# Kernel optimization log

Measured on AMD Instinct MI355X. Metric: run time of the kernel, lower is better.

The kernel has to match this reference:

```python
import jax, jax.numpy as jnp
import numpy as np

N = 6144
D = 128
TAU = 0.1
ADJ_P = 0.005  # edge density


def _l2_normalize(x, eps=1e-12):
    # matches torch F.normalize: x / max(||x||, eps)
    n = jnp.sqrt(jnp.sum(x * x, axis=-1, keepdims=True))
    return x / jnp.maximum(n, eps)


def setup_inputs() -> dict:
    key = jax.random.key(0)
    ks = jax.random.split(key, 8)
    embF = jax.random.normal(ks[0], (N, D), jnp.float32)
    embM = jax.random.normal(ks[1], (N, D), jnp.float32)
    embP = jax.random.normal(ks[2], (N, D), jnp.float32)
    FM_adj = (jax.random.uniform(ks[3], (N, N)) < ADJ_P).astype(jnp.float32)
    FP_adj = (jax.random.uniform(ks[4], (N, N)) < ADJ_P).astype(jnp.float32)
    W1 = jax.random.normal(ks[5], (2 * D, D), jnp.float32) * (1.0 / np.sqrt(2 * D))
    b1 = jnp.zeros((D,), jnp.float32)
    W2 = jax.random.normal(ks[6], (D, 2), jnp.float32) * (1.0 / np.sqrt(D))
    b2 = jnp.zeros((2,), jnp.float32)
    return {"embF": embF, "embM": embM, "embP": embP,
            "FM_adj": FM_adj, "FP_adj": FP_adj,
            "W1": W1, "b1": b1, "W2": W2, "b2": b2}


def reference(embF, embM, embP, FM_adj, FP_adj, W1, b1, W2, b2):
    # attention-weighted neighbor aggregation
    FM_repr = (FM_adj @ embM) / jnp.maximum(FM_adj.sum(1, keepdims=True), 1.0)
    FP_repr = (FP_adj @ embP) / jnp.maximum(FP_adj.sum(1, keepdims=True), 1.0)
    # stack(dim=1).view(N,-1) == concat along feature dim
    feat = jnp.concatenate([FM_repr, FP_repr], axis=1)            # [N, 2D]
    h = jnp.maximum(feat @ W1 + b1, 0.0)                           # ReLU (dropout inactive in eval)
    weights = jax.nn.softmax(h @ W2 + b2, axis=-1)                 # [N, 2]

    Fn = _l2_normalize(embF)
    Mn = _l2_normalize(embM)
    Pn = _l2_normalize(embP)

    FM_sim = jnp.exp((Fn @ Mn.T) / TAU)                            # [N, Nm]
    FP_sim = jnp.exp((Fn @ Pn.T) / TAU)                            # [N, Np]

    FM_pos = jnp.sum(FM_sim * FM_adj, axis=1)
    FP_pos = jnp.sum(FP_sim * FP_adj, axis=1)
    FM_neg = jnp.sum(FM_sim, axis=1) - FM_pos
    FP_neg = jnp.sum(FP_sim, axis=1) - FP_pos

    w0, w1w = weights[:, 0], weights[:, 1]
    wp = w0 * FM_pos + w1w * FP_pos
    wn = w0 * FM_neg + w1w * FP_neg

    nei_count = jnp.maximum(FM_adj.sum(1) + FP_adj.sum(1), 1.0)
    ratio = wp / (wp + wn) / nei_count
    ratio = jnp.maximum(ratio, 1e-10)
    loss = jnp.mean(-jnp.log(ratio))
    return loss, weights
```

## Files before the change

kernel.cpp:

```cpp
#include <hip/hip_runtime.h>
#include <hip/hip_bf16.h>

#define NN 6144
#define DD 128
#define PBL 136
#define INV_TAU 10.0f

typedef __attribute__((ext_vector_type(4))) float f32x4;
typedef __attribute__((ext_vector_type(8))) short s16x8;

__device__ __forceinline__ void ld4_async(const float4* p, float4& d) {
    asm volatile("global_load_dwordx4 %0, %1, off" : "=v"(d) : "v"(p));
}
__device__ __forceinline__ void vm_wait0() {
    asm volatile("s_waitcnt vmcnt(0)" ::: "memory");
}

__global__ void k_normalize(const float* __restrict__ embF,
                            const float* __restrict__ embM,
                            const float* __restrict__ embP,
                            float* __restrict__ Fn,
                            float* __restrict__ rnM, float* __restrict__ rnP,
                            __hip_bfloat16* __restrict__ Fnb,
                            __hip_bfloat16* __restrict__ Mnb,
                            __hip_bfloat16* __restrict__ Pnb) {
    int which = blockIdx.y;
    const float* src = which == 0 ? embF : (which == 1 ? embM : embP);
    __hip_bfloat16* dstb = which == 0 ? Fnb : (which == 1 ? Mnb : Pnb);
    int wave = threadIdx.x >> 6, lane = threadIdx.x & 63;
    int row = blockIdx.x * 4 + wave;
    float2 v = reinterpret_cast<const float2*>(src + (size_t)row * DD)[lane];
    float s = v.x * v.x + v.y * v.y;
#pragma unroll
    for (int m = 1; m <= 32; m <<= 1) s += __shfl_xor(s, m);
    float inv = 1.0f / fmaxf(sqrtf(s), 1e-12f);
    float2 o; o.x = v.x * inv; o.y = v.y * inv;
    if (which == 0)
        reinterpret_cast<float2*>(Fn + (size_t)row * DD)[lane] = o;
    if (lane == 0) {
        if (which == 1) rnM[row] = inv;
        if (which == 2) rnP[row] = inv;
    }
    __hip_bfloat162 ob;
    ob.x = __float2bfloat16(o.x);
    ob.y = __float2bfloat16(o.y);
    reinterpret_cast<__hip_bfloat162*>(dstb + (size_t)row * DD)[lane] = ob;
}

__device__ __forceinline__ void sparse_body(
        int unit, char* smem,
        const float* __restrict__ FM_adj, const float* __restrict__ FP_adj,
        const float* __restrict__ embM, const float* __restrict__ embP,
        const float* __restrict__ Fn,
        const float* __restrict__ rnM, const float* __restrict__ rnP,
        float* __restrict__ feat,
        float* __restrict__ FMpos, float* __restrict__ FPpos,
        float* __restrict__ cntF, float* __restrict__ cntP) {
    float* FnS = (float*)smem;
    int (*lbufT)[4] = (int(*)[4])(smem + 512);
    int* listS = (int*)(smem + 512 + 4096);
    float (*reprS)[DD] = (float(*)[DD])(smem + 512 + 4096 + 512);
    float* posS = (float*)(smem + 512 + 4096 + 512 + 4096);
    int* wvS = (int*)(smem + 512 + 4096 + 512 + 4096 + 32);
    int* Ktot = (int*)(smem + 512 + 4096 + 512 + 4096 + 32 + 16);

    const int row = unit >> 1, h = unit & 1;
    const float* adj  = h ? FP_adj : FM_adj;
    const float* embX = h ? embP : embM;
    const float* RN   = h ? rnP : rnM;
    const int tid = threadIdx.x, wv = tid >> 6, lane = tid & 63;

    if (tid < 32)
        reinterpret_cast<float4*>(FnS)[tid] =
            reinterpret_cast<const float4*>(Fn + (size_t)row * DD)[tid];

    const float4* rp = reinterpret_cast<const float4*>(adj + (size_t)row * NN);
    float4 v0, v1, v2, v3, v4, v5;
    ld4_async(rp + tid,        v0);
    ld4_async(rp + 256 + tid,  v1);
    ld4_async(rp + 512 + tid,  v2);
    ld4_async(rp + 768 + tid,  v3);
    ld4_async(rp + 1024 + tid, v4);
    ld4_async(rp + 1280 + tid, v5);
    vm_wait0();
    float4 vv[6] = {v0, v1, v2, v3, v4, v5};
    int mycnt = 0;
#pragma unroll
    for (int u = 0; u < 6; ++u) {
        int cb = (u * 256 + tid) * 4;
        if (vv[u].x != 0.f) { if (mycnt < 4) lbufT[tid][mycnt] = cb;     mycnt++; }
        if (vv[u].y != 0.f) { if (mycnt < 4) lbufT[tid][mycnt] = cb + 1; mycnt++; }
        if (vv[u].z != 0.f) { if (mycnt < 4) lbufT[tid][mycnt] = cb + 2; mycnt++; }
        if (vv[u].w != 0.f) { if (mycnt < 4) lbufT[tid][mycnt] = cb + 3; mycnt++; }
    }
    int cnt = mycnt < 4 ? mycnt : 4;
    int x = cnt;
#pragma unroll
    for (int d = 1; d < 64; d <<= 1) {
        int y = __shfl_up(x, d);
        if (lane >= d) x += y;
    }
    int t = mycnt;
#pragma unroll
    for (int msk = 1; msk <= 32; msk <<= 1) t += __shfl_xor(t, msk);
    if (tid == 0) Ktot[1] = 0;
    if (lane == 63) wvS[wv] = x;
    __syncthreads();
    if (lane == 0) atomicAdd(&Ktot[1], t);
    if (tid == 0) {
        int s = 0;
#pragma unroll
        for (int i = 0; i < 4; ++i) { int v = wvS[i]; wvS[i] = s; s += v; }
        Ktot[0] = s < 128 ? s : 128;
    }
    __syncthreads();
    int off = wvS[wv] + (x - cnt);
    for (int i = 0; i < cnt; ++i) {
        int s = off + i;
        if (s < 128) listS[s] = lbufT[tid][i];
    }
    __syncthreads();
    const int K = Ktot[0];
    const float trueK = (float)Ktot[1];

    const int hw = tid >> 5, sl = tid & 31;
    float4 f4 = reinterpret_cast<const float4*>(FnS)[sl];
    float4 racc = {0.f, 0.f, 0.f, 0.f};
    float wsum = 0.f;
    for (int k = hw; k < K; k += 8) {
        int j = listS[k];
        float rn = RN[j];
        float4 e = reinterpret_cast<const float4*>(embX + (size_t)j * DD)[sl];
        racc.x += e.x; racc.y += e.y; racc.z += e.z; racc.w += e.w;
        float d = f4.x * e.x + f4.y * e.y + f4.z * e.z + f4.w * e.w;
#pragma unroll
        for (int msk = 1; msk <= 16; msk <<= 1) d += __shfl_xor(d, msk);
        wsum += __expf(d * rn * INV_TAU);
    }
    reinterpret_cast<float4*>(&reprS[hw][0])[sl] = racc;
    if (sl == 0) posS[hw] = wsum;
    __syncthreads();
    if (tid < DD) {
        float s = 0.f;
#pragma unroll
        for (int i = 0; i < 8; ++i) s += reprS[i][tid];
        feat[(size_t)row * (2 * DD) + h * DD + tid] = s / fmaxf(trueK, 1.0f);
    }
    if (tid == 0) {
        float p = 0.f;
#pragma unroll
        for (int i = 0; i < 8; ++i) p += posS[i];
        (h ? FPpos : FMpos)[row] = p;
        (h ? cntP : cntF)[row] = trueK;
    }
}

__device__ __forceinline__ void dense_body(
        int unit, char* smem,
        const __hip_bfloat16* __restrict__ Fnb,
        const __hip_bfloat16* __restrict__ Mnb,
        const __hip_bfloat16* __restrict__ Pnb,
        float* __restrict__ FMtot, float* __restrict__ FPtot) {
    __hip_bfloat16 (*Bs)[PBL] = (__hip_bfloat16(*)[PBL])smem;
    const int bx = unit % 48, by = (unit / 48) % 16, half = unit / 768;
    const __hip_bfloat16* Bnb = half ? Pnb : Mnb;
    float* TOT = half ? FPtot : FMtot;
    const int tid = threadIdx.x;
    const int w = tid >> 6, lane = tid & 63;
    const int m = lane & 15, q = lane >> 4;
    const int rb = bx * 128 + w * 32;
    const int j0 = by * (NN / 16);

    s16x8 a[2][4];
#pragma unroll
    for (int g = 0; g < 2; ++g)
#pragma unroll
        for (int ks = 0; ks < 4; ++ks)
            a[g][ks] = *reinterpret_cast<const s16x8*>(
                Fnb + (size_t)(rb + g * 16 + m) * DD + ks * 32 + q * 8);

    float4 s0, s1, s2, s3;
    auto issue = [&](int jc) {
        const float4* gp = reinterpret_cast<const float4*>(Bnb + (size_t)jc * DD);
        ld4_async(gp + tid,       s0);
        ld4_async(gp + 256 + tid, s1);
        ld4_async(gp + 512 + tid, s2);
        ld4_async(gp + 768 + tid, s3);
    };
    auto stash = [&](int idx, const float4& v) {
        *reinterpret_cast<float4*>(&Bs[idx >> 4][(idx & 15) * 8]) = v;
    };

    issue(j0);
    float tot[2][4] = {{0.f, 0.f, 0.f, 0.f}, {0.f, 0.f, 0.f, 0.f}};
    for (int it = 0; it < 6; ++it) {
        vm_wait0();
        __syncthreads();
        stash(tid, s0);
        stash(256 + tid, s1);
        stash(512 + tid, s2);
        stash(768 + tid, s3);
        __syncthreads();
        if (it + 1 < 6) issue(j0 + (it + 1) * 64);
#pragma unroll
        for (int t = 0; t < 4; ++t) {
            s16x8 b[4];
#pragma unroll
            for (int ks = 0; ks < 4; ++ks)
                b[ks] = *reinterpret_cast<const s16x8*>(
                    &Bs[t * 16 + m][ks * 32 + q * 8]);
#pragma unroll
            for (int g = 0; g < 2; ++g) {
                f32x4 acc = {0.f, 0.f, 0.f, 0.f};
#pragma unroll
                for (int ks = 0; ks < 4; ++ks)
                    acc = __builtin_amdgcn_mfma_f32_16x16x32_bf16(
                        a[g][ks], b[ks], acc, 0, 0, 0);
#pragma unroll
                for (int r = 0; r < 4; ++r)
                    tot[g][r] += __expf(acc[r] * INV_TAU);
            }
        }
    }
#pragma unroll
    for (int msk = 1; msk <= 8; msk <<= 1)
#pragma unroll
        for (int g = 0; g < 2; ++g)
#pragma unroll
            for (int r = 0; r < 4; ++r)
                tot[g][r] += __shfl_xor(tot[g][r], msk);
    if (m == 0)
#pragma unroll
        for (int g = 0; g < 2; ++g)
#pragma unroll
            for (int r = 0; r < 4; ++r)
                atomicAdd(&TOT[rb + g * 16 + q * 4 + r], tot[g][r]);
}

__global__ __launch_bounds__(256) void k_main(
        const float* __restrict__ FM_adj, const float* __restrict__ FP_adj,
        const float* __restrict__ embM, const float* __restrict__ embP,
        const float* __restrict__ Fn,
        const float* __restrict__ rnM, const float* __restrict__ rnP,
        const __hip_bfloat16* __restrict__ Fnb,
        const __hip_bfloat16* __restrict__ Mnb,
        const __hip_bfloat16* __restrict__ Pnb,
        float* __restrict__ feat,
        float* __restrict__ FMpos, float* __restrict__ FPpos,
        float* __restrict__ FMtot, float* __restrict__ FPtot,
        float* __restrict__ cntF, float* __restrict__ cntP) {
    __shared__ char smem[64 * PBL * 2];
    const int b = blockIdx.x;
    const int u = b / 9, r = b - u * 9;
    if (r == 8)
        dense_body(u, smem, Fnb, Mnb, Pnb, FMtot, FPtot);
    else
        sparse_body(u * 8 + r, smem, FM_adj, FP_adj, embM, embP,
                    Fn, rnM, rnP, feat, FMpos, FPpos, cntF, cntP);
}

__global__ __launch_bounds__(256) void k_mlp(
        const float* __restrict__ feat,
        const float* __restrict__ W1, const float* __restrict__ b1,
        const float* __restrict__ W2, const float* __restrict__ b2,
        const float* __restrict__ FMpos, const float* __restrict__ FPpos,
        const float* __restrict__ FMtot, const float* __restrict__ FPtot,
        const float* __restrict__ cntF, const float* __restrict__ cntP,
        float* __restrict__ out) {
    __shared__ float featS[4][2 * DD];
    __shared__ float partS[2][4][DD];
    __shared__ float redS[2][4][2];
    __shared__ float lossS[4];
    const int tid = threadIdx.x;
    const int cp = tid >> 7, d = tid & 127;
    const int row0 = blockIdx.x * 4;
    for (int idx = tid; idx < 4 * 2 * DD; idx += 256)
        featS[idx >> 8][idx & 255] = feat[(size_t)row0 * (2 * DD) + idx];
    __syncthreads();
    float bb = (cp == 0) ? b1[d] : 0.f;
    float acc[4];
#pragma unroll
    for (int r = 0; r < 4; ++r) acc[r] = bb;
    const int c0 = cp * 128;
    for (int c = c0; c < c0 + 128; c += 2) {
        float wA = W1[c * DD + d];
        float wB = W1[(c + 1) * DD + d];
#pragma unroll
        for (int r = 0; r < 4; ++r)
            acc[r] = fmaf(featS[r][c + 1], wB, fmaf(featS[r][c], wA, acc[r]));
    }
#pragma unroll
    for (int r = 0; r < 4; ++r) partS[cp][r][d] = acc[r];
    __syncthreads();
    if (tid < 128) {
        const int lane = tid & 63, wv = tid >> 6;
        float w20 = W2[2 * tid], w21 = W2[2 * tid + 1];
        float p0s[4], p1s[4];
#pragma unroll
        for (int r = 0; r < 4; ++r) {
            float hh = fmaxf(partS[0][r][tid] + partS[1][r][tid], 0.f);
            p0s[r] = hh * w20;
            p1s[r] = hh * w21;
        }
#pragma unroll
        for (int r = 0; r < 4; ++r)
#pragma unroll
            for (int msk = 1; msk <= 32; msk <<= 1) {
                p0s[r] += __shfl_xor(p0s[r], msk);
                p1s[r] += __shfl_xor(p1s[r], msk);
            }
        if (lane == 0)
#pragma unroll
            for (int r = 0; r < 4; ++r) {
                redS[wv][r][0] = p0s[r];
                redS[wv][r][1] = p1s[r];
            }
    }
    __syncthreads();
    if (tid < 4) {
        int row = row0 + tid;
        float z0 = redS[0][tid][0] + redS[1][tid][0] + b2[0];
        float z1 = redS[0][tid][1] + redS[1][tid][1] + b2[1];
        float mx = fmaxf(z0, z1);
        float e0 = expf(z0 - mx), e1 = expf(z1 - mx);
        float inv = 1.0f / (e0 + e1);
        float w0 = e0 * inv, w1 = e1 * inv;
        out[1 + row * 2 + 0] = w0;
        out[1 + row * 2 + 1] = w1;
        float wp = w0 * FMpos[row] + w1 * FPpos[row];
        float wn = w0 * (FMtot[row] - FMpos[row]) +
                   w1 * (FPtot[row] - FPpos[row]);
        float nei = fmaxf(cntF[row] + cntP[row], 1.0f);
        float ratio = wp / (wp + wn) / nei;
        ratio = fmaxf(ratio, 1e-10f);
        lossS[tid] = -logf(ratio);
    }
    __syncthreads();
    if (tid == 0) {
        float L = 0.f;
#pragma unroll
        for (int r = 0; r < 4; ++r) L += lossS[r];
        atomicAdd(out, L * (1.0f / NN));
    }
}

extern "C" void kernel_launch(void* const* d_in, const int* in_sizes, int n_in,
                              void* d_out, int out_size, void* d_ws, size_t ws_size,
                              hipStream_t stream) {
    const float* embF   = (const float*)d_in[0];
    const float* embM   = (const float*)d_in[1];
    const float* embP   = (const float*)d_in[2];
    const float* FM_adj = (const float*)d_in[3];
    const float* FP_adj = (const float*)d_in[4];
    const float* W1     = (const float*)d_in[5];
    const float* b1     = (const float*)d_in[6];
    const float* W2     = (const float*)d_in[7];
    const float* b2     = (const float*)d_in[8];
    float* out = (float*)d_out;

    float* ws = (float*)d_ws;
    float* FMtot = ws;
    float* FPtot = FMtot + NN;
    float* FMpos = FPtot + NN;
    float* FPpos = FMpos + NN;
    float* cntF  = FPpos + NN;
    float* cntP  = cntF + NN;
    float* rnM   = cntP + NN;
    float* rnP   = rnM + NN;
    float* feat  = rnP + NN;
    float* Fn    = feat + (size_t)NN * 2 * DD;
    __hip_bfloat16* Fnb = (__hip_bfloat16*)(Fn + (size_t)NN * DD);
    __hip_bfloat16* Mnb = Fnb + (size_t)NN * DD;
    __hip_bfloat16* Pnb = Mnb + (size_t)NN * DD;

    hipMemsetAsync(FMtot, 0, 2 * NN * sizeof(float), stream);
    hipMemsetAsync(d_out, 0, sizeof(float), stream);

    k_normalize<<<dim3(NN / 4, 3), 256, 0, stream>>>(embF, embM, embP,
                                                     Fn, rnM, rnP,
                                                     Fnb, Mnb, Pnb);
    k_main<<<dim3(13824), 256, 0, stream>>>(FM_adj, FP_adj, embM, embP,
                                            Fn, rnM, rnP, Fnb, Mnb, Pnb,
                                            feat, FMpos, FPpos, FMtot, FPtot,
                                            cntF, cntP);
    k_mlp<<<dim3(NN / 4), 256, 0, stream>>>(feat, W1, b1, W2, b2,
                                            FMpos, FPpos, FMtot, FPtot,
                                            cntF, cntP, out);
}
```

Baseline: 384.2 us.

## Run the MLP layer on bf16 MFMA and split out the loss kernel

Replaces the scalar FP32 feat@W1 MLP kernel with a bf16 MFMA 16x16x32 kernel. feat is now stored as bf16 and W1 is pre-transposed to bf16 in a small prep kernel. The second linear layer is reduced through shuffles and atomics into a z buffer, and a separate loss kernel then does the softmax and loss reduction. The lbufT shared layout is also widened from 4 to 5 ints per entry. The aim is to cut the cost of the MLP stage, which was a small share of the runtime. In exchange it adds bf16 rounding to feat and W1, two extra launches, and atomic accumulation.

Measured after the change: 369.4 us. 3.9% less time.

```diff
diff --git a/kernel.cpp b/kernel.cpp
--- a/kernel.cpp
+++ b/kernel.cpp
@@ -47,22 +47,28 @@
     reinterpret_cast<__hip_bfloat162*>(dstb + (size_t)row * DD)[lane] = ob;
 }
 
+__global__ void k_prep(const float* __restrict__ W1,
+                       __hip_bfloat16* __restrict__ W1tb) {
+    int n = blockIdx.x, c = threadIdx.x;
+    W1tb[n * 256 + c] = __float2bfloat16(W1[c * DD + n]);
+}
+
 __device__ __forceinline__ void sparse_body(
         int unit, char* smem,
         const float* __restrict__ FM_adj, const float* __restrict__ FP_adj,
         const float* __restrict__ embM, const float* __restrict__ embP,
         const float* __restrict__ Fn,
         const float* __restrict__ rnM, const float* __restrict__ rnP,
-        float* __restrict__ feat,
+        __hip_bfloat16* __restrict__ featb,
         float* __restrict__ FMpos, float* __restrict__ FPpos,
         float* __restrict__ cntF, float* __restrict__ cntP) {
     float* FnS = (float*)smem;
-    int (*lbufT)[4] = (int(*)[4])(smem + 512);
-    int* listS = (int*)(smem + 512 + 4096);
-    float (*reprS)[DD] = (float(*)[DD])(smem + 512 + 4096 + 512);
-    float* posS = (float*)(smem + 512 + 4096 + 512 + 4096);
-    int* wvS = (int*)(smem + 512 + 4096 + 512 + 4096 + 32);
-    int* Ktot = (int*)(smem + 512 + 4096 + 512 + 4096 + 32 + 16);
+    int (*lbufT)[5] = (int(*)[5])(smem + 512);
+    int* listS = (int*)(smem + 512 + 5120);
+    float (*reprS)[DD] = (float(*)[DD])(smem + 512 + 5120 + 512);
+    float* posS = (float*)(smem + 512 + 5120 + 512 + 4096);
+    int* wvS = (int*)(smem + 512 + 5120 + 512 + 4096 + 32);
+    int* Ktot = (int*)(smem + 512 + 5120 + 512 + 4096 + 32 + 16);
 
     const int row = unit >> 1, h = unit & 1;
     const float* adj  = h ? FP_adj : FM_adj;
@@ -144,7 +150,8 @@
         float s = 0.f;
 #pragma unroll
         for (int i = 0; i < 8; ++i) s += reprS[i][tid];
-        feat[(size_t)row * (2 * DD) + h * DD + tid] = s / fmaxf(trueK, 1.0f);
+        featb[(size_t)row * (2 * DD) + h * DD + tid] =
+            __float2bfloat16(s / fmaxf(trueK, 1.0f));
     }
     if (tid == 0) {
         float p = 0.f;
@@ -245,7 +252,7 @@
         const __hip_bfloat16* __restrict__ Fnb,
         const __hip_bfloat16* __restrict__ Mnb,
         const __hip_bfloat16* __restrict__ Pnb,
-        float* __restrict__ feat,
+        __hip_bfloat16* __restrict__ featb,
         float* __restrict__ FMpos, float* __restrict__ FPpos,
         float* __restrict__ FMtot, float* __restrict__ FPtot,
         float* __restrict__ cntF, float* __restrict__ cntP) {
@@ -256,92 +263,74 @@
         dense_body(u, smem, Fnb, Mnb, Pnb, FMtot, FPtot);
     else
         sparse_body(u * 8 + r, smem, FM_adj, FP_adj, embM, embP,
-                    Fn, rnM, rnP, feat, FMpos, FPpos, cntF, cntP);
-}
-
-__global__ __launch_bounds__(256) void k_mlp(
-        const float* __restrict__ feat,
-        const float* __restrict__ W1, const float* __restrict__ b1,
-        const float* __restrict__ W2, const float* __restrict__ b2,
-        const float* __restrict__ FMpos, const float* __restrict__ FPpos,
-        const float* __restrict__ FMtot, const float* __restrict__ FPtot,
-        const float* __restrict__ cntF, const float* __restrict__ cntP,
-        float* __restrict__ out) {
-    __shared__ float featS[4][2 * DD];
-    __shared__ float partS[2][4][DD];
-    __shared__ float redS[2][4][2];
-    __shared__ float lossS[4];
+                    Fn, rnM, rnP, featb, FMpos, FPpos, cntF, cntP);
+}
+
+__global__ __launch_bounds__(256) void k_mlp2(
+        const __hip_bfloat16* __restrict__ featb,
+        const __hip_bfloat16* __restrict__ W1tb,
+        const float* __restrict__ b1, const float* __restrict__ W2,
+        float* __restrict__ z) {
+    const int tid = threadIdx.x, w = tid >> 6, lane = tid & 63;
+    const int m = lane & 15, q = lane >> 4;
+    const int unit = blockIdx.x * 4 + w;
+    const int rb = (unit >> 3) * 16, n0 = (unit & 7) * 16;
+    f32x4 acc = {0.f, 0.f, 0.f, 0.f};
+#pragma unroll
+    for (int ks = 0; ks < 8; ++ks) {
+        s16x8 a = *reinterpret_cast<const s16x8*>(
+            featb + (size_t)(rb + m) * 256 + ks * 32 + q * 8);
+        s16x8 b = *reinterpret_cast<const s16x8*>(
+            W1tb + (size_t)(n0 + m) * 256 + ks * 32 + q * 8);
+        acc = __builtin_amdgcn_mfma_f32_16x16x32_bf16(a, b, acc, 0, 0, 0);
+    }
+    const int n = n0 + m;
+    float bias = b1[n], w20 = W2[2 * n], w21 = W2[2 * n + 1];
+#pragma unroll
+    for (int r = 0; r < 4; ++r) {
+        float h = fmaxf(acc[r] + bias, 0.f);
+        float p0 = h * w20, p1 = h * w21;
+#pragma unroll
+        for (int msk = 1; msk <= 8; msk <<= 1) {
+            p0 += __shfl_xor(p0, msk);
+            p1 += __shfl_xor(p1, msk);
+        }
+        if (m == 0) {
+            int row = rb + q * 4 + r;
+            atomicAdd(&z[2 * row], p0);
+            atomicAdd(&z[2 * row + 1], p1);
+        }
+    }
+}
+
+__global__ void k_loss(const float* __restrict__ z, const float* __restrict__ b2,
+                       const float* __restrict__ FMpos, const float* __restrict__ FPpos,
+                       const float* __restrict__ FMtot, const float* __restrict__ FPtot,
+                       const float* __restrict__ cntF, const float* __restrict__ cntP,
+                       float* __restrict__ out) {
+    __shared__ float red[4];
     const int tid = threadIdx.x;
-    const int cp = tid >> 7, d = tid & 127;
-    const int row0 = blockIdx.x * 4;
-    for (int idx = tid; idx < 4 * 2 * DD; idx += 256)
-        featS[idx >> 8][idx & 255] = feat[(size_t)row0 * (2 * DD) + idx];
-    __syncthreads();
-    float bb = (cp == 0) ? b1[d] : 0.f;
-    float acc[4];
-#pragma unroll
-    for (int r = 0; r < 4; ++r) acc[r] = bb;
-    const int c0 = cp * 128;
-    for (int c = c0; c < c0 + 128; c += 2) {
-        float wA = W1[c * DD + d];
-        float wB = W1[(c + 1) * DD + d];
-#pragma unroll
-        for (int r = 0; r < 4; ++r)
-            acc[r] = fmaf(featS[r][c + 1], wB, fmaf(featS[r][c], wA, acc[r]));
-    }
-#pragma unroll
-    for (int r = 0; r < 4; ++r) partS[cp][r][d] = acc[r];
-    __syncthreads();
-    if (tid < 128) {
-        const int lane = tid & 63, wv = tid >> 6;
-        float w20 = W2[2 * tid], w21 = W2[2 * tid + 1];
-        float p0s[4], p1s[4];
-#pragma unroll
-        for (int r = 0; r < 4; ++r) {
-            float hh = fmaxf(partS[0][r][tid] + partS[1][r][tid], 0.f);
-            p0s[r] = hh * w20;
-            p1s[r] = hh * w21;
-        }
-#pragma unroll
-        for (int r = 0; r < 4; ++r)
-#pragma unroll
-            for (int msk = 1; msk <= 32; msk <<= 1) {
-                p0s[r] += __shfl_xor(p0s[r], msk);
-                p1s[r] += __shfl_xor(p1s[r], msk);
-            }
-        if (lane == 0)
-#pragma unroll
-            for (int r = 0; r < 4; ++r) {
-                redS[wv][r][0] = p0s[r];
-                redS[wv][r][1] = p1s[r];
-            }
-    }
-    __syncthreads();
-    if (tid < 4) {
-        int row = row0 + tid;
-        float z0 = redS[0][tid][0] + redS[1][tid][0] + b2[0];
-        float z1 = redS[0][tid][1] + redS[1][tid][1] + b2[1];
-        float mx = fmaxf(z0, z1);
-        float e0 = expf(z0 - mx), e1 = expf(z1 - mx);
-        float inv = 1.0f / (e0 + e1);
-        float w0 = e0 * inv, w1 = e1 * inv;
-        out[1 + row * 2 + 0] = w0;
-        out[1 + row * 2 + 1] = w1;
-        float wp = w0 * FMpos[row] + w1 * FPpos[row];
-        float wn = w0 * (FMtot[row] - FMpos[row]) +
-                   w1 * (FPtot[row] - FPpos[row]);
-        float nei = fmaxf(cntF[row] + cntP[row], 1.0f);
-        float ratio = wp / (wp + wn) / nei;
-        ratio = fmaxf(ratio, 1e-10f);
-        lossS[tid] = -logf(ratio);
-    }
-    __syncthreads();
-    if (tid == 0) {
-        float L = 0.f;
-#pragma unroll
-        for (int r = 0; r < 4; ++r) L += lossS[r];
-        atomicAdd(out, L * (1.0f / NN));
-    }
+    const int lane = tid & 63, wv = tid >> 6;
+    const int row = blockIdx.x * 256 + tid;
+    float z0 = z[row * 2] + b2[0], z1 = z[row * 2 + 1] + b2[1];
+    float mx = fmaxf(z0, z1);
+    float e0 = expf(z0 - mx), e1 = expf(z1 - mx);
+    float inv = 1.0f / (e0 + e1);
+    float w0 = e0 * inv, w1 = e1 * inv;
+    out[1 + row * 2 + 0] = w0;
+    out[1 + row * 2 + 1] = w1;
+    float wp = w0 * FMpos[row] + w1 * FPpos[row];
+    float wn = w0 * (FMtot[row] - FMpos[row]) + w1 * (FPtot[row] - FPpos[row]);
+    float nei = fmaxf(cntF[row] + cntP[row], 1.0f);
+    float ratio = wp / (wp + wn) / nei;
+    ratio = fmaxf(ratio, 1e-10f);
+    float term = -logf(ratio);
+#pragma unroll
+    for (int msk = 1; msk <= 32; msk <<= 1) term += __shfl_xor(term, msk);
+    if (lane == 0) red[wv] = term;
+    __syncthreads();
+    if (tid == 0)
+        atomicAdd(out, (red[0] + red[1] + red[2] + red[3]) * (1.0f / NN));
 }
 
 extern "C" void kernel_launch(void* const* d_in, const int* in_sizes, int n_in,
@@ -361,29 +350,32 @@
     float* ws = (float*)d_ws;
     float* FMtot = ws;
     float* FPtot = FMtot + NN;
-    float* FMpos = FPtot + NN;
+    float* zbuf  = FPtot + NN;
+    float* FMpos = zbuf + 2 * NN;
     float* FPpos = FMpos + NN;
     float* cntF  = FPpos + NN;
     float* cntP  = cntF + NN;
     float* rnM   = cntP + NN;
     float* rnP   = rnM + NN;
-    float* feat  = rnP + NN;
-    float* Fn    = feat + (size_t)NN * 2 * DD;
+    float* Fn    = rnP + NN;
     __hip_bfloat16* Fnb = (__hip_bfloat16*)(Fn + (size_t)NN * DD);
     __hip_bfloat16* Mnb = Fnb + (size_t)NN * DD;
     __hip_bfloat16* Pnb = Mnb + (size_t)NN * DD;
-
-    hipMemsetAsync(FMtot, 0, 2 * NN * sizeof(float), stream);
+    __hip_bfloat16* featb = Pnb + (size_t)NN * DD;
+    __hip_bfloat16* W1tb  = featb + (size_t)NN * 256;
+
+    hipMemsetAsync(FMtot, 0, 4 * NN * sizeof(float), stream);
     hipMemsetAsync(d_out, 0, sizeof(float), stream);
 
     k_normalize<<<dim3(NN / 4, 3), 256, 0, stream>>>(embF, embM, embP,
                                                      Fn, rnM, rnP,
                                                      Fnb, Mnb, Pnb);
+    k_prep<<<dim3(128), 256, 0, stream>>>(W1, W1tb);
     k_main<<<dim3(13824), 256, 0, stream>>>(FM_adj, FP_adj, embM, embP,
                                             Fn, rnM, rnP, Fnb, Mnb, Pnb,
-                                            feat, FMpos, FPpos, FMtot, FPtot,
+                                            featb, FMpos, FPpos, FMtot, FPtot,
                                             cntF, cntP);
-    k_mlp<<<dim3(NN / 4), 256, 0, stream>>>(feat, W1, b1, W2, b2,
-                                            FMpos, FPpos, FMtot, FPtot,
-                                            cntF, cntP, out);
-}
+    k_mlp2<<<dim3(768), 256, 0, stream>>>(featb, W1tb, b1, W2, zbuf);
+    k_loss<<<dim3(NN / 256), 256, 0, stream>>>(zbuf, b2, FMpos, FPpos,
+                                               FMtot, FPtot, cntF, cntP, out);
+}
```
